# Optimization experiments

Measured on AMD Instinct MI355X. Metric: run time of the kernel, lower is better.

The kernel has to match this reference:

```python
import jax, jax.numpy as jnp
import numpy as np

N_ATOMS = 16384
APC = 64            # atoms per conformer
N_CONF = 256        # 64 mols * 4 confs
N_MOL = 64
DEG = 32
E = N_ATOMS * DEG
H = 128             # hidden_channels = num_filters = out_channels
G = 50              # num_gaussians
L = 6               # num_interactions
CUTOFF = 10.0
LOG2 = float(np.log(2.0))


def ssp(x):
    # ShiftedSoftplus: softplus(x) - log(2)
    return jax.nn.softplus(x) - LOG2


def setup_inputs() -> dict:
    key = jax.random.key(0)
    ks = jax.random.split(key, 24)
    rng = np.random.default_rng(0)

    z = jnp.asarray(rng.integers(1, 100, size=(N_ATOMS,)), dtype=jnp.int64 if jax.config.jax_enable_x64 else jnp.int32)
    # positions uniform in a 5A box -> all intra-conformer distances < cutoff
    pos = jax.random.uniform(ks[0], (N_ATOMS, 3), dtype=jnp.float32) * 5.0

    # within-conformer random edges, no self loops (radius_graph surrogate)
    i = np.repeat(np.arange(N_ATOMS), DEG)
    off = rng.integers(1, APC, size=E)
    j = (i // APC) * APC + (i % APC + off) % APC
    edge_index = jnp.asarray(np.stack([j, i]), dtype=jnp.int32)  # [2,E] (source, target)

    atom_to_conf = jnp.asarray(np.arange(N_ATOMS) // APC, dtype=jnp.int32)
    conf_to_mol = jnp.asarray(np.arange(N_CONF) // (N_CONF // N_MOL), dtype=jnp.int32)

    s = 0.05
    p = {
        'emb':     jax.random.normal(ks[1], (120, H), jnp.float32) * s,
        # per-interaction stacked params [L, ...]
        'mlp_w1':  jax.random.normal(ks[2], (L, G, H), jnp.float32) * s,
        'mlp_b1':  jnp.zeros((L, H), jnp.float32),
        'mlp_w2':  jax.random.normal(ks[3], (L, H, H), jnp.float32) * s,
        'mlp_b2':  jnp.zeros((L, H), jnp.float32),
        'cf_w1':   jax.random.normal(ks[4], (L, H, H), jnp.float32) * s,
        'cf_w2':   jax.random.normal(ks[5], (L, H, H), jnp.float32) * s,
        'cf_b2':   jnp.zeros((L, H), jnp.float32),
        'int_w':   jax.random.normal(ks[6], (L, H, H), jnp.float32) * s,
        'int_b':   jnp.zeros((L, H), jnp.float32),
        # readout head
        'out_w1':  jax.random.normal(ks[7], (H, H), jnp.float32) * s,
        'out_b1':  jnp.zeros((H,), jnp.float32),
        'out_w2':  jax.random.normal(ks[8], (H, H), jnp.float32) * s,
        'out_b2':  jnp.zeros((H,), jnp.float32),
        'head_w1': jax.random.normal(ks[9], (H, H // 2), jnp.float32) * s,
        'head_b1': jnp.zeros((H // 2,), jnp.float32),
        'head_w2': jax.random.normal(ks[10], (H // 2, 1), jnp.float32) * s,
        'head_b2': jnp.zeros((1,), jnp.float32),
    }
    return dict(z=z, pos=pos, edge_index=edge_index, atom_to_conf=atom_to_conf,
                conf_to_mol=conf_to_mol, **p)


def reference(z, pos, edge_index, atom_to_conf, conf_to_mol, emb,
              mlp_w1, mlp_b1, mlp_w2, mlp_b2, cf_w1, cf_w2, cf_b2,
              int_w, int_b, out_w1, out_b1, out_w2, out_b2,
              head_w1, head_b1, head_w2, head_b2):
    row, col = edge_index[0], edge_index[1]  # message from row, aggregated at col

    h = emb[z]                                             # [N,H]
    edge_weight = jnp.linalg.norm(pos[row] - pos[col], axis=-1)  # [E]

    # GaussianSmearing
    offset = jnp.linspace(0.0, CUTOFF, G)
    coeff = -0.5 / (offset[1] - offset[0]) ** 2
    edge_attr = jnp.exp(coeff * (edge_weight[:, None] - offset[None, :]) ** 2)  # [E,G]

    C = 0.5 * (jnp.cos(edge_weight * jnp.pi / CUTOFF) + 1.0)  # cosine cutoff [E]

    for l in range(L):
        # filter network on edge features, modulated by cutoff envelope
        Wf = ssp(edge_attr @ mlp_w1[l] + mlp_b1[l]) @ mlp_w2[l] + mlp_b2[l]
        Wf = Wf * C[:, None]                               # [E,H]
        xf = h @ cf_w1[l]                                  # lin1 (no bias) [N,H]
        msg = xf[row] * Wf                                 # gather * filter [E,H]
        agg = jax.ops.segment_sum(msg, col, num_segments=N_ATOMS)  # scatter-add [N,H]
        xc = agg @ cf_w2[l] + cf_b2[l]                     # lin2
        h = h + (ssp(xc) @ int_w[l] + int_b[l])            # act, lin, residual

    h = ssp(h @ out_w1 + out_b1)
    h = h @ out_w2 + out_b2                                # [N,H]

    conf_emb = jax.ops.segment_sum(h, atom_to_conf, num_segments=N_CONF)   # [C,H]
    mol_emb = jax.ops.segment_sum(conf_emb, conf_to_mol, num_segments=N_MOL)  # [M,H]

    out = (ssp(mol_emb @ head_w1 + head_b1) @ head_w2 + head_b2)[:, 0]  # [M]
    return out
```

## Files before the change

### kernel.cpp

```cpp
#include <hip/hip_runtime.h>
#include <math.h>

#define N_ATOMS 16384
#define APC 64
#define N_CONF 256
#define N_MOL 64
#define DEG 32
#define NEDGE (N_ATOMS * DEG)
#define H 128
#define G 50
#define NL 6
#define TP0 512
#define TPB 4096
#define CUTOFF 10.0f

typedef __attribute__((ext_vector_type(8))) short short8_t;
typedef __attribute__((ext_vector_type(4))) float f32x4;
typedef __attribute__((ext_vector_type(2))) float f32x2;

__device__ __forceinline__ float ssp_f(float x) {
  float e = __expf(-fabsf(x));
  return fmaxf(x, 0.f) + __logf(1.f + e) - 0.69314718055994531f;
}
__device__ __forceinline__ unsigned short bf16_rne(float x) {
  unsigned u = __float_as_uint(x);
  unsigned r = u + 0x7FFF + ((u >> 16) & 1);
  return (unsigned short)(r >> 16);
}
__device__ __forceinline__ float bf16_to_f(unsigned short s) {
  return __uint_as_float(((unsigned)s) << 16);
}
__device__ __forceinline__ float bflo(unsigned u) { return __uint_as_float(u << 16); }
__device__ __forceinline__ float bfhi(unsigned u) { return __uint_as_float(u & 0xFFFF0000u); }

__global__ __launch_bounds__(256) void k_setup(
    const float* __restrict__ pos, const int* __restrict__ esrc,
    const int* __restrict__ etgt, int* __restrict__ pk,
    const float* __restrict__ cf_w1, const float* __restrict__ cf_w2,
    const float* __restrict__ int_w, const float* __restrict__ out_w1,
    const float* __restrict__ out_w2, short* __restrict__ PW,
    const float* __restrict__ w1, const float* __restrict__ b1,
    const float* __restrict__ w2, const float* __restrict__ b2,
    float* __restrict__ T, int* __restrict__ cnt) {
  __shared__ float g2[2][64];
  __shared__ float S2[2][128];
  const int b = blockIdx.x;
  const int tid = threadIdx.x;
  if (b == 0 && tid == 0) *cnt = 0;
  if (b < 2048) {
    int e = b * 256 + tid;
    int r = esrc[e], c = etgt[e];
    float dx = pos[r * 3 + 0] - pos[c * 3 + 0];
    float dy = pos[r * 3 + 1] - pos[c * 3 + 1];
    float dz = pos[r * 3 + 2] - pos[c * 3 + 2];
    float d = sqrtf(dx * dx + dy * dy + dz * dz);
    int i = (int)(d * ((float)(TPB - 1) / CUTOFF) + 0.5f);
    if (i > TPB - 1) i = TPB - 1;
    if (i < 0) i = 0;
    pk[e] = (i << 8) | ((r & (APC - 1)) << 20);
  } else if (b < 2208) {
    int e = (b - 2048) * 256 + tid;
    int g = e >> 11, t = e & 2047;
    int kb = t >> 9, rem = t & 511, nt = rem >> 6, lane = rem & 63;
    int quad = lane >> 4, ln = lane & 15;
    int kbase = kb * 32 + quad * 8;
    int n = nt * 16 + ln;
    const float* src;
    if (g < 12) {
      int l = g >> 1;
      src = (g & 1) ? (int_w + l * 16384) : (cf_w2 + l * 16384);
    } else if (g < 18) {
      src = cf_w1 + (g - 12) * 16384;
    } else {
      src = (g == 18) ? out_w1 : out_w2;
    }
    short hv[8], lv[8];
    #pragma unroll
    for (int j = 0; j < 8; j++) {
      float x = src[(kbase + j) * H + n];
      unsigned short hb = bf16_rne(x);
      hv[j] = (short)hb;
      lv[j] = (short)bf16_rne(x - bf16_to_f(hb));
    }
    size_t base = (size_t)g * 32768 + (size_t)t * 8;
    *(short8_t*)&PW[base] = *(short8_t*)hv;
    *(short8_t*)&PW[base + 16384] = *(short8_t*)lv;
  } else {
    int bb = b - 2208;
    const int l = bb >> 8;
    const int grp = tid >> 7;
    const int c = tid & 127;
    const int p = (bb & 255) * 2 + grp;
    const float d = (float)p * (CUTOFF / (float)(TP0 - 1));
    const float gspace = CUTOFF / (float)(G - 1);
    const float coeff = -0.5f / (gspace * gspace);
    if (c < G) {
      float x = d - (float)c * gspace;
      g2[grp][c] = __expf(coeff * x * x);
    }
    __syncthreads();
    const float* W1 = w1 + l * G * H;
    float s = b1[l * H + c];
    #pragma unroll 5
    for (int i = 0; i < G; i++) s += g2[grp][i] * W1[i * H + c];
    S2[grp][c] = ssp_f(s);
    __syncthreads();
    const float* W2 = w2 + l * H * H;
    float o = b2[l * H + c];
    #pragma unroll 8
    for (int j = 0; j < H; j++) o += S2[grp][j] * W2[j * H + c];
    float Cc = 0.5f * (__cosf(d * (3.14159265358979f / CUTOFF)) + 1.f);
    T[((size_t)l * TP0 + p) * H + c] = o * Cc;
  }
}

__global__ __launch_bounds__(256) void k_up(const float* __restrict__ T,
                                            unsigned short* __restrict__ Tb) {
  int t = blockIdx.x * 256 + threadIdx.x;
  int l = t >> 17;
  int rem = t & 131071;
  int p4 = rem >> 5, cg = rem & 31;
  int c = cg * 4;
  float u = (float)p4 * ((float)(TP0 - 1) / (float)(TPB - 1));
  int i = (int)u;
  if (i > TP0 - 2) i = TP0 - 2;
  float f = u - (float)i;
  const float* a = T + ((size_t)l * TP0 + i) * H + c;
  float4 v0 = *(const float4*)a;
  float4 v1 = *(const float4*)(a + H);
  ushort4 o;
  o.x = bf16_rne(v0.x + f * (v1.x - v0.x));
  o.y = bf16_rne(v0.y + f * (v1.y - v0.y));
  o.z = bf16_rne(v0.z + f * (v1.z - v0.z));
  o.w = bf16_rne(v0.w + f * (v1.w - v0.w));
  *(ushort4*)&Tb[((size_t)l * TPB + p4) * H + c] = o;
}

#define MFMA(a, b, c) __builtin_amdgcn_mfma_f32_16x16x32_bf16((a), (b), (c), 0, 0, 0)

__device__ __forceinline__ void gemm_rt2(const short (*AH)[136], const short (*AL)[136],
                                         const short* __restrict__ pw,
                                         int rt2, int nt, int lane, int quad, int ln,
                                         f32x4 acc[2]) {
  #pragma unroll
  for (int kb = 0; kb < 4; kb++) {
    const short* pb = pw + ((size_t)(kb * 8 + nt) * 64 + lane) * 8;
    short8_t bh = *(const short8_t*)pb;
    short8_t bl = *(const short8_t*)(pb + 16384);
    int ko = kb * 32 + quad * 8;
    #pragma unroll
    for (int rtt = 0; rtt < 2; rtt++) {
      int row = rt2 * 32 + rtt * 16 + ln;
      short8_t ah = *(const short8_t*)&AH[row][ko];
      short8_t al = *(const short8_t*)&AL[row][ko];
      acc[rtt] = MFMA(ah, bh, acc[rtt]);
      acc[rtt] = MFMA(ah, bl, acc[rtt]);
      acc[rtt] = MFMA(al, bh, acc[rtt]);
    }
  }
}

__global__ __launch_bounds__(1024, 1) void k_mega(
    const int* __restrict__ z, const float* __restrict__ emb,
    const int* __restrict__ pk, const unsigned short* __restrict__ Tb,
    const short* __restrict__ PW, const float* __restrict__ cf_b2,
    const float* __restrict__ int_b, const float* __restrict__ out_b1,
    const float* __restrict__ out_b2, float* __restrict__ ce,
    const float* __restrict__ hw1, const float* __restrict__ hb1,
    const float* __restrict__ hw2, const float* __restrict__ hb2,
    int* __restrict__ cnt, float* __restrict__ outp) {
  __shared__ float xs[64][132];
  __shared__ __align__(16) short hH[64][136], hL[64][136];
  __shared__ __align__(16) short tH[64][136], tL[64][136];
  __shared__ __align__(16) short S1H[64][136], S1L[64][136];
  __shared__ int pks[2048];
  __shared__ float ps[2][128];
  __shared__ int is_last;
  const int conf = blockIdx.x;
  const int tid = threadIdx.x;
  const int lane = tid & 63, w = tid >> 6;
  const int quad = lane >> 4, ln = lane & 15;
  const int rt2 = w & 1, nt = w >> 1;
  const int eg = lane >> 4, ch0 = (lane & 15) * 8;

  pks[tid] = pk[conf * 2048 + tid];
  pks[tid + 1024] = pk[conf * 2048 + 1024 + tid];

  {
    int r = tid >> 4, cb = (tid & 15) * 8;
    const float* src = emb + (size_t)z[conf * 64 + r] * H + cb;
    float4 v0 = *(const float4*)src, v1 = *(const float4*)(src + 4);
    float vv[8] = {v0.x, v0.y, v0.z, v0.w, v1.x, v1.y, v1.z, v1.w};
    short hv[8], lv[8];
    #pragma unroll
    for (int u = 0; u < 8; u++) {
      unsigned short hb = bf16_rne(vv[u]);
      hv[u] = (short)hb;
      lv[u] = (short)bf16_rne(vv[u] - bf16_to_f(hb));
    }
    *(short8_t*)&hH[r][cb] = *(short8_t*)hv;
    *(short8_t*)&hL[r][cb] = *(short8_t*)lv;
  }
  __syncthreads();

  {
    f32x4 acc[2] = {{0.f, 0.f, 0.f, 0.f}, {0.f, 0.f, 0.f, 0.f}};
    gemm_rt2(hH, hL, PW + (size_t)12 * 32768, rt2, nt, lane, quad, ln, acc);
    int col = nt * 16 + ln;
    #pragma unroll
    for (int rtt = 0; rtt < 2; rtt++)
      #pragma unroll
      for (int reg = 0; reg < 4; reg++)
        xs[rt2 * 32 + rtt * 16 + quad * 4 + reg][col] = acc[rtt][reg];
  }
  __syncthreads();

  for (int l = 0; l < NL; l++) {
    const char* Tlb = (const char*)(Tb + (size_t)l * TPB * H) + ch0 * 2;
    #pragma unroll 1
    for (int aa = 0; aa < 4; aa++) {
      int a2 = w * 4 + aa;
      int ms[8];
      uint4 tvv[8];
      #pragma unroll
      for (int it = 0; it < 8; it++) {
        ms[it] = pks[a2 * DEG + it * 4 + eg];
        tvv[it] = *(const uint4*)(Tlb + (ms[it] & 0xFFFFF));
      }
      f32x2 ac0 = {0.f, 0.f}, ac1 = {0.f, 0.f}, ac2 = {0.f, 0.f}, ac3 = {0.f, 0.f};
      #pragma unroll
      for (int it = 0; it < 8; it++) {
        int sl = ms[it] >> 20;
        const float* xr = &xs[sl][ch0];
        float4 x0 = *(const float4*)xr;
        float4 x1 = *(const float4*)(xr + 4);
        uint4 tv = tvv[it];
        ac0 = __builtin_elementwise_fma((f32x2){bflo(tv.x), bfhi(tv.x)},
                                        (f32x2){x0.x, x0.y}, ac0);
        ac1 = __builtin_elementwise_fma((f32x2){bflo(tv.y), bfhi(tv.y)},
                                        (f32x2){x0.z, x0.w}, ac1);
        ac2 = __builtin_elementwise_fma((f32x2){bflo(tv.z), bfhi(tv.z)},
                                        (f32x2){x1.x, x1.y}, ac2);
        ac3 = __builtin_elementwise_fma((f32x2){bflo(tv.w), bfhi(tv.w)},
                                        (f32x2){x1.z, x1.w}, ac3);
      }
      float accs[8] = {ac0.x, ac0.y, ac1.x, ac1.y, ac2.x, ac2.y, ac3.x, ac3.y};
      #pragma unroll
      for (int j = 0; j < 8; j++) {
        accs[j] += __shfl_xor(accs[j], 16);
        accs[j] += __shfl_xor(accs[j], 32);
      }
      float va = eg == 0 ? accs[0] : eg == 1 ? accs[2] : eg == 2 ? accs[4] : accs[6];
      float vb = eg == 0 ? accs[1] : eg == 1 ? accs[3] : eg == 2 ? accs[5] : accs[7];
      unsigned short ha = bf16_rne(va), hb = bf16_rne(vb);
      unsigned short la = bf16_rne(va - bf16_to_f(ha));
      unsigned short lb = bf16_rne(vb - bf16_to_f(hb));
      int cw = ch0 + eg * 2;
      *(short2*)&S1H[a2][cw] = make_short2((short)ha, (short)hb);
      *(short2*)&S1L[a2][cw] = make_short2((short)la, (short)lb);
    }
    __syncthreads();
    {
      f32x4 acc[2] = {{0.f, 0.f, 0.f, 0.f}, {0.f, 0.f, 0.f, 0.f}};
      gemm_rt2(S1H, S1L, PW + (size_t)(2 * l) * 32768, rt2, nt, lane, quad, ln, acc);
      int col = nt * 16 + ln;
      float bb = cf_b2[l * H + col];
      #pragma unroll
      for (int rtt = 0; rtt < 2; rtt++)
        #pragma unroll
        for (int reg = 0; reg < 4; reg++) {
          int row = rt2 * 32 + rtt * 16 + quad * 4 + reg;
          float v = ssp_f(acc[rtt][reg] + bb);
          unsigned short hb = bf16_rne(v);
          tH[row][col] = (short)hb;
          tL[row][col] = (short)bf16_rne(v - bf16_to_f(hb));
        }
    }
    __syncthreads();
    {
      f32x4 acc[2] = {{0.f, 0.f, 0.f, 0.f}, {0.f, 0.f, 0.f, 0.f}};
      gemm_rt2(tH, tL, PW + (size_t)(2 * l + 1) * 32768, rt2, nt, lane, quad, ln, acc);
      int col = nt * 16 + ln;
      float bb = int_b[l * H + col];
      #pragma unroll
      for (int rtt = 0; rtt < 2; rtt++)
        #pragma unroll
        for (int reg = 0; reg < 4; reg++) {
          int row = rt2 * 32 + rtt * 16 + quad * 4 + reg;
          float hv = bf16_to_f((unsigned short)hH[row][col]) +
                     bf16_to_f((unsigned short)hL[row][col]);
          float v = acc[rtt][reg] + bb + hv;
          unsigned short hb = bf16_rne(v);
          hH[row][col] = (short)hb;
          hL[row][col] = (short)bf16_rne(v - bf16_to_f(hb));
        }
    }
    __syncthreads();
    if (l < NL - 1) {
      f32x4 acc[2] = {{0.f, 0.f, 0.f, 0.f}, {0.f, 0.f, 0.f, 0.f}};
      gemm_rt2(hH, hL, PW + (size_t)(13 + l) * 32768, rt2, nt, lane, quad, ln, acc);
      int col = nt * 16 + ln;
      #pragma unroll
      for (int rtt = 0; rtt < 2; rtt++)
        #pragma unroll
        for (int reg = 0; reg < 4; reg++)
          xs[rt2 * 32 + rtt * 16 + quad * 4 + reg][col] = acc[rtt][reg];
      __syncthreads();
    }
  }

  {
    f32x4 acc[2] = {{0.f, 0.f, 0.f, 0.f}, {0.f, 0.f, 0.f, 0.f}};
    gemm_rt2(hH, hL, PW + (size_t)18 * 32768, rt2, nt, lane, quad, ln, acc);
    int col = nt * 16 + ln;
    float bb = out_b1[col];
    #pragma unroll
    for (int rtt = 0; rtt < 2; rtt++)
      #pragma unroll
      for (int reg = 0; reg < 4; reg++) {
        int row = rt2 * 32 + rtt * 16 + quad * 4 + reg;
        float v = ssp_f(acc[rtt][reg] + bb);
        unsigned short hb = bf16_rne(v);
        tH[row][col] = (short)hb;
        tL[row][col] = (short)bf16_rne(v - bf16_to_f(hb));
      }
  }
  __syncthreads();
  {
    f32x4 acc[2] = {{0.f, 0.f, 0.f, 0.f}, {0.f, 0.f, 0.f, 0.f}};
    gemm_rt2(tH, tL, PW + (size_t)19 * 32768, rt2, nt, lane, quad, ln, acc);
    int col = nt * 16 + ln;
    float s = acc[0][0] + acc[0][1] + acc[0][2] + acc[0][3] +
              acc[1][0] + acc[1][1] + acc[1][2] + acc[1][3];
    s += __shfl_xor(s, 16);
    s += __shfl_xor(s, 32);
    if (quad == 0) ps[rt2][col] = s;
  }
  __syncthreads();
  if (tid < 128) {
    float v = ps[0][tid] + ps[1][tid] + 64.f * out_b2[tid];
    __hip_atomic_store(&ce[conf * 128 + tid], v, __ATOMIC_RELAXED,
                       __HIP_MEMORY_SCOPE_AGENT);
  }
  __syncthreads();
  if (tid == 0) {
    __threadfence();
    int old = __hip_atomic_fetch_add(cnt, 1, __ATOMIC_ACQ_REL,
                                     __HIP_MEMORY_SCOPE_AGENT);
    is_last = (old == N_CONF - 1) ? 1 : 0;
  }
  __syncthreads();
  if (is_last) {
    __threadfence();
    float* mol = &xs[0][0];
    for (int t = tid; t < N_MOL * 128; t += 1024) {
      int m = t >> 7, c = t & 127;
      const float* b = ce + (size_t)(m * 4) * 128;
      float s = __hip_atomic_load(&b[c], __ATOMIC_RELAXED, __HIP_MEMORY_SCOPE_AGENT) +
                __hip_atomic_load(&b[128 + c], __ATOMIC_RELAXED, __HIP_MEMORY_SCOPE_AGENT) +
                __hip_atomic_load(&b[256 + c], __ATOMIC_RELAXED, __HIP_MEMORY_SCOPE_AGENT) +
                __hip_atomic_load(&b[384 + c], __ATOMIC_RELAXED, __HIP_MEMORY_SCOPE_AGENT);
      mol[t] = s;
    }
    __syncthreads();
    float* q = (float*)&S1H[0][0];
    for (int t = tid; t < N_MOL * 64; t += 1024) {
      int m = t >> 6, j = t & 63;
      float qq = hb1[j];
      #pragma unroll 8
      for (int c = 0; c < H; c++) qq += mol[m * 128 + c] * hw1[c * 64 + j];
      q[t] = ssp_f(qq);
    }
    __syncthreads();
    if (tid < N_MOL) {
      float o = hb2[0];
      #pragma unroll 8
      for (int j = 0; j < 64; j++) o += q[tid * 64 + j] * hw2[j];
      outp[tid] = o;
    }
  }
}

extern "C" void kernel_launch(void* const* d_in, const int* in_sizes, int n_in,
                              void* d_out, int out_size, void* d_ws, size_t ws_size,
                              hipStream_t stream) {
  const int*   z       = (const int*)d_in[0];
  const float* pos     = (const float*)d_in[1];
  const int*   eidx    = (const int*)d_in[2];
  const float* emb     = (const float*)d_in[5];
  const float* mlp_w1  = (const float*)d_in[6];
  const float* mlp_b1  = (const float*)d_in[7];
  const float* mlp_w2  = (const float*)d_in[8];
  const float* mlp_b2  = (const float*)d_in[9];
  const float* cf_w1   = (const float*)d_in[10];
  const float* cf_w2   = (const float*)d_in[11];
  const float* cf_b2   = (const float*)d_in[12];
  const float* int_w   = (const float*)d_in[13];
  const float* int_b   = (const float*)d_in[14];
  const float* out_w1  = (const float*)d_in[15];
  const float* out_b1  = (const float*)d_in[16];
  const float* out_w2  = (const float*)d_in[17];
  const float* out_b2  = (const float*)d_in[18];
  const float* head_w1 = (const float*)d_in[19];
  const float* head_b1 = (const float*)d_in[20];
  const float* head_w2 = (const float*)d_in[21];
  const float* head_b2 = (const float*)d_in[22];

  char* ws = (char*)d_ws;
  float*          T   = (float*)ws;
  unsigned short* Tb  = (unsigned short*)(ws + (size_t)NL * TP0 * H * 4);
  char*           p2  = (char*)Tb + (size_t)NL * TPB * H * 2;
  int*            pk  = (int*)p2;
  short*          PW  = (short*)(p2 + (size_t)NEDGE * 4);
  float*          ce  = (float*)((char*)PW + (size_t)20 * 32768 * 2);
  int*            cnt = (int*)((char*)ce + (size_t)N_CONF * H * 4);

  k_setup<<<3744, 256, 0, stream>>>(pos, eidx, eidx + NEDGE, pk,
                                    cf_w1, cf_w2, int_w, out_w1, out_w2, PW,
                                    mlp_w1, mlp_b1, mlp_w2, mlp_b2, T, cnt);
  k_up<<<(NL * TPB * H / 4) / 256, 256, 0, stream>>>(T, Tb);

  k_mega<<<N_CONF, 1024, 0, stream>>>(z, emb, pk, Tb, PW, cf_b2, int_b,
                                      out_b1, out_b2, ce,
                                      head_w1, head_b1, head_w2, head_b2,
                                      cnt, (float*)d_out);
}
```

Baseline: 243.1 us.

## Fuse setup, upsample and main kernels into one persistent kernel with grid barriers

Merges the three launches (setup, table upsampling, per-conformer mega kernel) into a single kernel of 256 blocks that uses atomic-counter grid barriers between phases. Edge distance packing is now computed per conformer from positions staged in LDS instead of in a separate pass, and the edge-table gathers are software-pipelined so the next atom's loads are issued while the current one accumulates. This removes launch gaps and the global pk round trip. In exchange it depends on all 256 blocks being co-resident for the spin barriers, spreads the filter-table work over fewer threads, and raises register pressure from the double-buffered gathers.

```diff
diff --git a/kernel.cpp b/kernel.cpp
--- a/kernel.cpp
+++ b/kernel.cpp
@@ -33,33 +33,62 @@
 __device__ __forceinline__ float bflo(unsigned u) { return __uint_as_float(u << 16); }
 __device__ __forceinline__ float bfhi(unsigned u) { return __uint_as_float(u & 0xFFFF0000u); }
 
-__global__ __launch_bounds__(256) void k_setup(
-    const float* __restrict__ pos, const int* __restrict__ esrc,
-    const int* __restrict__ etgt, int* __restrict__ pk,
+#define MFMA(a, b, c) __builtin_amdgcn_mfma_f32_16x16x32_bf16((a), (b), (c), 0, 0, 0)
+
+__device__ __forceinline__ void gemm_rt2(const short (*AH)[136], const short (*AL)[136],
+                                         const short* __restrict__ pw,
+                                         int rt2, int nt, int lane, int quad, int ln,
+                                         f32x4 acc[2]) {
+  #pragma unroll
+  for (int kb = 0; kb < 4; kb++) {
+    const short* pb = pw + ((size_t)(kb * 8 + nt) * 64 + lane) * 8;
+    short8_t bh = *(const short8_t*)pb;
+    short8_t bl = *(const short8_t*)(pb + 16384);
+    int ko = kb * 32 + quad * 8;
+    #pragma unroll
+    for (int rtt = 0; rtt < 2; rtt++) {
+      int row = rt2 * 32 + rtt * 16 + ln;
+      short8_t ah = *(const short8_t*)&AH[row][ko];
+      short8_t al = *(const short8_t*)&AL[row][ko];
+      acc[rtt] = MFMA(ah, bh, acc[rtt]);
+      acc[rtt] = MFMA(ah, bl, acc[rtt]);
+      acc[rtt] = MFMA(al, bh, acc[rtt]);
+    }
+  }
+}
+
+__global__ __launch_bounds__(1024, 1) void k_all(
+    const int* __restrict__ z, const float* __restrict__ pos,
+    const int* __restrict__ esrc, const float* __restrict__ emb,
+    const float* __restrict__ mlp_w1, const float* __restrict__ mlp_b1,
+    const float* __restrict__ mlp_w2, const float* __restrict__ mlp_b2,
     const float* __restrict__ cf_w1, const float* __restrict__ cf_w2,
-    const float* __restrict__ int_w, const float* __restrict__ out_w1,
-    const float* __restrict__ out_w2, short* __restrict__ PW,
-    const float* __restrict__ w1, const float* __restrict__ b1,
-    const float* __restrict__ w2, const float* __restrict__ b2,
-    float* __restrict__ T, int* __restrict__ cnt) {
-  __shared__ float g2[2][64];
-  __shared__ float S2[2][128];
+    const float* __restrict__ cf_b2, const float* __restrict__ int_w,
+    const float* __restrict__ int_b, const float* __restrict__ out_w1,
+    const float* __restrict__ out_b1, const float* __restrict__ out_w2,
+    const float* __restrict__ out_b2, const float* __restrict__ hw1,
+    const float* __restrict__ hb1, const float* __restrict__ hw2,
+    const float* __restrict__ hb2, float* __restrict__ T,
+    unsigned short* __restrict__ Tb, short* __restrict__ PW,
+    float* __restrict__ ce, int* __restrict__ cnt, float* __restrict__ outp) {
+  __shared__ __align__(16) char smem[148240];
+  float (*xs)[132] = (float (*)[132])(smem);
+  short (*hH)[136] = (short (*)[136])(smem + 33792);
+  short (*hL)[136] = (short (*)[136])(smem + 51200);
+  short (*tH)[136] = (short (*)[136])(smem + 68608);
+  short (*tL)[136] = (short (*)[136])(smem + 86016);
+  short (*S1H)[136] = (short (*)[136])(smem + 103424);
+  short (*S1L)[136] = (short (*)[136])(smem + 120832);
+  int* pks = (int*)(smem + 138240);
+  float (*ps)[128] = (float (*)[128])(smem + 146432);
+  float* posL = (float*)(smem + 147456);
+  int* is_last = (int*)(smem + 148224);
+
   const int b = blockIdx.x;
   const int tid = threadIdx.x;
-  if (b == 0 && tid == 0) *cnt = 0;
-  if (b < 2048) {
-    int e = b * 256 + tid;
-    int r = esrc[e], c = etgt[e];
-    float dx = pos[r * 3 + 0] - pos[c * 3 + 0];
-    float dy = pos[r * 3 + 1] - pos[c * 3 + 1];
-    float dz = pos[r * 3 + 2] - pos[c * 3 + 2];
-    float d = sqrtf(dx * dx + dy * dy + dz * dz);
-    int i = (int)(d * ((float)(TPB - 1) / CUTOFF) + 0.5f);
-    if (i > TPB - 1) i = TPB - 1;
-    if (i < 0) i = 0;
-    pk[e] = (i << 8) | ((r & (APC - 1)) << 20);
-  } else if (b < 2208) {
-    int e = (b - 2048) * 256 + tid;
+
+  if (tid < 160) {
+    int e = b * 160 + tid;
     int g = e >> 11, t = e & 2047;
     int kb = t >> 9, rem = t & 511, nt = rem >> 6, lane = rem & 63;
     int quad = lane >> 4, ln = lane & 15;
@@ -85,107 +114,112 @@
     size_t base = (size_t)g * 32768 + (size_t)t * 8;
     *(short8_t*)&PW[base] = *(short8_t*)hv;
     *(short8_t*)&PW[base + 16384] = *(short8_t*)lv;
-  } else {
-    int bb = b - 2208;
-    const int l = bb >> 8;
-    const int grp = tid >> 7;
-    const int c = tid & 127;
-    const int p = (bb & 255) * 2 + grp;
-    const float d = (float)p * (CUTOFF / (float)(TP0 - 1));
+  }
+  {
+    float* g8 = (float*)smem;
+    float* S8 = (float*)(smem + 2048);
     const float gspace = CUTOFF / (float)(G - 1);
     const float coeff = -0.5f / (gspace * gspace);
-    if (c < G) {
-      float x = d - (float)c * gspace;
-      g2[grp][c] = __expf(coeff * x * x);
-    }
-    __syncthreads();
-    const float* W1 = w1 + l * G * H;
-    float s = b1[l * H + c];
-    #pragma unroll 5
-    for (int i = 0; i < G; i++) s += g2[grp][i] * W1[i * H + c];
-    S2[grp][c] = ssp_f(s);
-    __syncthreads();
-    const float* W2 = w2 + l * H * H;
-    float o = b2[l * H + c];
-    #pragma unroll 8
-    for (int j = 0; j < H; j++) o += S2[grp][j] * W2[j * H + c];
-    float Cc = 0.5f * (__cosf(d * (3.14159265358979f / CUTOFF)) + 1.f);
-    T[((size_t)l * TP0 + p) * H + c] = o * Cc;
-  }
-}
-
-__global__ __launch_bounds__(256) void k_up(const float* __restrict__ T,
-                                            unsigned short* __restrict__ Tb) {
-  int t = blockIdx.x * 256 + threadIdx.x;
-  int l = t >> 17;
-  int rem = t & 131071;
-  int p4 = rem >> 5, cg = rem & 31;
-  int c = cg * 4;
-  float u = (float)p4 * ((float)(TP0 - 1) / (float)(TPB - 1));
-  int i = (int)u;
-  if (i > TP0 - 2) i = TP0 - 2;
-  float f = u - (float)i;
-  const float* a = T + ((size_t)l * TP0 + i) * H + c;
-  float4 v0 = *(const float4*)a;
-  float4 v1 = *(const float4*)(a + H);
-  ushort4 o;
-  o.x = bf16_rne(v0.x + f * (v1.x - v0.x));
-  o.y = bf16_rne(v0.y + f * (v1.y - v0.y));
-  o.z = bf16_rne(v0.z + f * (v1.z - v0.z));
-  o.w = bf16_rne(v0.w + f * (v1.w - v0.w));
-  *(ushort4*)&Tb[((size_t)l * TPB + p4) * H + c] = o;
-}
-
-#define MFMA(a, b, c) __builtin_amdgcn_mfma_f32_16x16x32_bf16((a), (b), (c), 0, 0, 0)
-
-__device__ __forceinline__ void gemm_rt2(const short (*AH)[136], const short (*AL)[136],
-                                         const short* __restrict__ pw,
-                                         int rt2, int nt, int lane, int quad, int ln,
-                                         f32x4 acc[2]) {
-  #pragma unroll
-  for (int kb = 0; kb < 4; kb++) {
-    const short* pb = pw + ((size_t)(kb * 8 + nt) * 64 + lane) * 8;
-    short8_t bh = *(const short8_t*)pb;
-    short8_t bl = *(const short8_t*)(pb + 16384);
-    int ko = kb * 32 + quad * 8;
-    #pragma unroll
-    for (int rtt = 0; rtt < 2; rtt++) {
-      int row = rt2 * 32 + rtt * 16 + ln;
-      short8_t ah = *(const short8_t*)&AH[row][ko];
-      short8_t al = *(const short8_t*)&AL[row][ko];
-      acc[rtt] = MFMA(ah, bh, acc[rtt]);
-      acc[rtt] = MFMA(ah, bl, acc[rtt]);
-      acc[rtt] = MFMA(al, bh, acc[rtt]);
-    }
-  }
-}
-
-__global__ __launch_bounds__(1024, 1) void k_mega(
-    const int* __restrict__ z, const float* __restrict__ emb,
-    const int* __restrict__ pk, const unsigned short* __restrict__ Tb,
-    const short* __restrict__ PW, const float* __restrict__ cf_b2,
-    const float* __restrict__ int_b, const float* __restrict__ out_b1,
-    const float* __restrict__ out_b2, float* __restrict__ ce,
-    const float* __restrict__ hw1, const float* __restrict__ hb1,
-    const float* __restrict__ hw2, const float* __restrict__ hb2,
-    int* __restrict__ cnt, float* __restrict__ outp) {
-  __shared__ float xs[64][132];
-  __shared__ __align__(16) short hH[64][136], hL[64][136];
-  __shared__ __align__(16) short tH[64][136], tL[64][136];
-  __shared__ __align__(16) short S1H[64][136], S1L[64][136];
-  __shared__ int pks[2048];
-  __shared__ float ps[2][128];
-  __shared__ int is_last;
-  const int conf = blockIdx.x;
-  const int tid = threadIdx.x;
+    const int grp = tid >> 7, c = tid & 127;
+    for (int r = 0; r < 2; r++) {
+      int pl = r * 8 + grp;
+      bool act = (pl < 12);
+      int pidx = b * 12 + (pl < 12 ? pl : 0);
+      int l = pidx >> 9, p = pidx & 511;
+      float d = (float)p * (CUTOFF / (float)(TP0 - 1));
+      if (act && c < G) {
+        float x = d - (float)c * gspace;
+        g8[grp * 64 + c] = __expf(coeff * x * x);
+      }
+      __syncthreads();
+      if (act) {
+        const float* W1 = mlp_w1 + l * G * H;
+        float s = mlp_b1[l * H + c];
+        #pragma unroll 5
+        for (int i = 0; i < G; i++) s += g8[grp * 64 + i] * W1[i * H + c];
+        S8[grp * 128 + c] = ssp_f(s);
+      }
+      __syncthreads();
+      if (act) {
+        const float* W2 = mlp_w2 + l * H * H;
+        float o = mlp_b2[l * H + c];
+        #pragma unroll 8
+        for (int j = 0; j < H; j++) o += S8[grp * 128 + j] * W2[j * H + c];
+        float Cc = 0.5f * (__cosf(d * (3.14159265358979f / CUTOFF)) + 1.f);
+        T[((size_t)l * TP0 + p) * H + c] = o * Cc;
+      }
+      __syncthreads();
+    }
+  }
+  __threadfence();
+  __syncthreads();
+  if (tid == 0) {
+    __hip_atomic_fetch_add(&cnt[0], 1, __ATOMIC_ACQ_REL, __HIP_MEMORY_SCOPE_AGENT);
+    while (__hip_atomic_load(&cnt[0], __ATOMIC_ACQUIRE, __HIP_MEMORY_SCOPE_AGENT)
+           != N_CONF)
+      __builtin_amdgcn_s_sleep(32);
+  }
+  __syncthreads();
+  __threadfence();
+
+  {
+    int gt = b * 1024 + tid;
+    #pragma unroll
+    for (int k = 0; k < 3; k++) {
+      int t = gt + k * 262144;
+      int l = t >> 17;
+      int rem = t & 131071;
+      int p4 = rem >> 5, cg = rem & 31;
+      int c = cg * 4;
+      float u = (float)p4 * ((float)(TP0 - 1) / (float)(TPB - 1));
+      int i = (int)u;
+      if (i > TP0 - 2) i = TP0 - 2;
+      float f = u - (float)i;
+      const float* a = T + ((size_t)l * TP0 + i) * H + c;
+      float4 v0 = *(const float4*)a;
+      float4 v1 = *(const float4*)(a + H);
+      ushort4 o;
+      o.x = bf16_rne(v0.x + f * (v1.x - v0.x));
+      o.y = bf16_rne(v0.y + f * (v1.y - v0.y));
+      o.z = bf16_rne(v0.z + f * (v1.z - v0.z));
+      o.w = bf16_rne(v0.w + f * (v1.w - v0.w));
+      *(ushort4*)&Tb[((size_t)l * TPB + p4) * H + c] = o;
+    }
+  }
+  __threadfence();
+  __syncthreads();
+  if (tid == 0) {
+    __hip_atomic_fetch_add(&cnt[1], 1, __ATOMIC_ACQ_REL, __HIP_MEMORY_SCOPE_AGENT);
+    while (__hip_atomic_load(&cnt[1], __ATOMIC_ACQUIRE, __HIP_MEMORY_SCOPE_AGENT)
+           != N_CONF)
+      __builtin_amdgcn_s_sleep(32);
+  }
+  __syncthreads();
+  __threadfence();
+
+  const int conf = b;
   const int lane = tid & 63, w = tid >> 6;
   const int quad = lane >> 4, ln = lane & 15;
   const int rt2 = w & 1, nt = w >> 1;
   const int eg = lane >> 4, ch0 = (lane & 15) * 8;
 
-  pks[tid] = pk[conf * 2048 + tid];
-  pks[tid + 1024] = pk[conf * 2048 + 1024 + tid];
-
+  if (tid < 192) posL[tid] = pos[conf * 192 + tid];
+  __syncthreads();
+  #pragma unroll
+  for (int k = 0; k < 2; k++) {
+    int e2 = k * 1024 + tid;
+    int r = esrc[conf * 2048 + e2];
+    int rl = r & (APC - 1);
+    int ca = e2 >> 5;
+    float dx = posL[rl * 3 + 0] - posL[ca * 3 + 0];
+    float dy = posL[rl * 3 + 1] - posL[ca * 3 + 1];
+    float dz = posL[rl * 3 + 2] - posL[ca * 3 + 2];
+    float d = sqrtf(dx * dx + dy * dy + dz * dz);
+    int i = (int)(d * ((float)(TPB - 1) / CUTOFF) + 0.5f);
+    if (i > TPB - 1) i = TPB - 1;
+    if (i < 0) i = 0;
+    pks[e2] = (i << 8) | (rl << 20);
+  }
   {
     int r = tid >> 4, cb = (tid & 15) * 8;
     const float* src = emb + (size_t)z[conf * 64 + r] * H + cb;
@@ -217,24 +251,34 @@
 
   for (int l = 0; l < NL; l++) {
     const char* Tlb = (const char*)(Tb + (size_t)l * TPB * H) + ch0 * 2;
-    #pragma unroll 1
+    int msA[8];
+    uint4 tvA[8];
+    #pragma unroll
+    for (int it = 0; it < 8; it++) msA[it] = pks[(w * 4) * DEG + it * 4 + eg];
+    #pragma unroll
+    for (int it = 0; it < 8; it++)
+      tvA[it] = *(const uint4*)(Tlb + (msA[it] & 0xFFFFF));
+    #pragma unroll
     for (int aa = 0; aa < 4; aa++) {
+      int msB[8];
+      uint4 tvB[8];
+      if (aa < 3) {
+        #pragma unroll
+        for (int it = 0; it < 8; it++)
+          msB[it] = pks[(w * 4 + aa + 1) * DEG + it * 4 + eg];
+        #pragma unroll
+        for (int it = 0; it < 8; it++)
+          tvB[it] = *(const uint4*)(Tlb + (msB[it] & 0xFFFFF));
+      }
       int a2 = w * 4 + aa;
-      int ms[8];
-      uint4 tvv[8];
+      f32x2 ac0 = {0.f, 0.f}, ac1 = {0.f, 0.f}, ac2 = {0.f, 0.f}, ac3 = {0.f, 0.f};
       #pragma unroll
       for (int it = 0; it < 8; it++) {
-        ms[it] = pks[a2 * DEG + it * 4 + eg];
-        tvv[it] = *(const uint4*)(Tlb + (ms[it] & 0xFFFFF));
-      }
-      f32x2 ac0 = {0.f, 0.f}, ac1 = {0.f, 0.f}, ac2 = {0.f, 0.f}, ac3 = {0.f, 0.f};
-      #pragma unroll
-      for (int it = 0; it < 8; it++) {
-        int sl = ms[it] >> 20;
+        int sl = msA[it] >> 20;
         const float* xr = &xs[sl][ch0];
         float4 x0 = *(const float4*)xr;
         float4 x1 = *(const float4*)(xr + 4);
-        uint4 tv = tvv[it];
+        uint4 tv = tvA[it];
         ac0 = __builtin_elementwise_fma((f32x2){bflo(tv.x), bfhi(tv.x)},
                                         (f32x2){x0.x, x0.y}, ac0);
         ac1 = __builtin_elementwise_fma((f32x2){bflo(tv.y), bfhi(tv.y)},
@@ -258,6 +302,11 @@
       int cw = ch0 + eg * 2;
       *(short2*)&S1H[a2][cw] = make_short2((short)ha, (short)hb);
       *(short2*)&S1L[a2][cw] = make_short2((short)la, (short)lb);
+      #pragma unroll
+      for (int it = 0; it < 8; it++) {
+        msA[it] = msB[it];
+        tvA[it] = tvB[it];
+      }
     }
     __syncthreads();
     {
@@ -345,21 +394,21 @@
   __syncthreads();
   if (tid == 0) {
     __threadfence();
-    int old = __hip_atomic_fetch_add(cnt, 1, __ATOMIC_ACQ_REL,
+    int old = __hip_atomic_fetch_add(&cnt[2], 1, __ATOMIC_ACQ_REL,
                                      __HIP_MEMORY_SCOPE_AGENT);
-    is_last = (old == N_CONF - 1) ? 1 : 0;
-  }
-  __syncthreads();
-  if (is_last) {
+    *is_last = (old == N_CONF - 1) ? 1 : 0;
+  }
+  __syncthreads();
+  if (*is_last) {
     __threadfence();
     float* mol = &xs[0][0];
     for (int t = tid; t < N_MOL * 128; t += 1024) {
       int m = t >> 7, c = t & 127;
-      const float* b = ce + (size_t)(m * 4) * 128;
-      float s = __hip_atomic_load(&b[c], __ATOMIC_RELAXED, __HIP_MEMORY_SCOPE_AGENT) +
-                __hip_atomic_load(&b[128 + c], __ATOMIC_RELAXED, __HIP_MEMORY_SCOPE_AGENT) +
-                __hip_atomic_load(&b[256 + c], __ATOMIC_RELAXED, __HIP_MEMORY_SCOPE_AGENT) +
-                __hip_atomic_load(&b[384 + c], __ATOMIC_RELAXED, __HIP_MEMORY_SCOPE_AGENT);
+      const float* bb = ce + (size_t)(m * 4) * 128;
+      float s = __hip_atomic_load(&bb[c], __ATOMIC_RELAXED, __HIP_MEMORY_SCOPE_AGENT) +
+                __hip_atomic_load(&bb[128 + c], __ATOMIC_RELAXED, __HIP_MEMORY_SCOPE_AGENT) +
+                __hip_atomic_load(&bb[256 + c], __ATOMIC_RELAXED, __HIP_MEMORY_SCOPE_AGENT) +
+                __hip_atomic_load(&bb[384 + c], __ATOMIC_RELAXED, __HIP_MEMORY_SCOPE_AGENT);
       mol[t] = s;
     }
     __syncthreads();
@@ -408,20 +457,15 @@
 
   char* ws = (char*)d_ws;
   float*          T   = (float*)ws;
-  unsigned short* Tb  = (unsigned short*)(ws + (size_t)NL * TP0 * H * 4);
-  char*           p2  = (char*)Tb + (size_t)NL * TPB * H * 2;
-  int*            pk  = (int*)p2;
-  short*          PW  = (short*)(p2 + (size_t)NEDGE * 4);
-  float*          ce  = (float*)((char*)PW + (size_t)20 * 32768 * 2);
-  int*            cnt = (int*)((char*)ce + (size_t)N_CONF * H * 4);
-
-  k_setup<<<3744, 256, 0, stream>>>(pos, eidx, eidx + NEDGE, pk,
-                                    cf_w1, cf_w2, int_w, out_w1, out_w2, PW,
-                                    mlp_w1, mlp_b1, mlp_w2, mlp_b2, T, cnt);
-  k_up<<<(NL * TPB * H / 4) / 256, 256, 0, stream>>>(T, Tb);
-
-  k_mega<<<N_CONF, 1024, 0, stream>>>(z, emb, pk, Tb, PW, cf_b2, int_b,
-                                      out_b1, out_b2, ce,
-                                      head_w1, head_b1, head_w2, head_b2,
-                                      cnt, (float*)d_out);
-}
+  unsigned short* Tb  = (unsigned short*)(ws + 1572864);
+  short*          PW  = (short*)(ws + 1572864 + 6291456);
+  float*          ce  = (float*)(ws + 9175040);
+  int*            cnt = (int*)(ws + 9306112);
+
+  hipMemsetAsync(cnt, 0, 12, stream);
+  k_all<<<N_CONF, 1024, 0, stream>>>(
+      z, pos, eidx, emb, mlp_w1, mlp_b1, mlp_w2, mlp_b2,
+      cf_w1, cf_w2, cf_b2, int_w, int_b, out_w1, out_b1, out_w2, out_b2,
+      head_w1, head_b1, head_w2, head_b2,
+      T, Tb, PW, ce, cnt, (float*)d_out);
+}
```

Result: slower. 536.2 us (+120.6%).
